# Kernel tuning notes

Measured on AMD Instinct MI355X. Metric: run time of the kernel, lower is better.

Reference implementation:

```python
import jax, jax.numpy as jnp
import numpy as np

G, D, F, B, T = 8, 20, 160, 64, 2000  # groups, dims(hidden), feature=G*D, batch, time


def _lstm_layer(x, Wih, Whh, bih, bhh):
    # x: [B, T, Din]; Wih: [4H, Din]; Whh: [4H, H]; PyTorch gate order i,f,g,o
    H = Whh.shape[1]
    xw = jnp.einsum('btd,gd->btg', x, Wih) + bih + bhh  # [B, T, 4H]
    xw = jnp.swapaxes(xw, 0, 1)  # [T, B, 4H]
    h0 = jnp.zeros((x.shape[0], H), x.dtype)

    def step(carry, xw_t):
        h, c = carry
        gates = xw_t + h @ Whh.T
        i, f, g, o = jnp.split(gates, 4, axis=-1)
        c = jax.nn.sigmoid(f) * c + jax.nn.sigmoid(i) * jnp.tanh(g)
        h = jax.nn.sigmoid(o) * jnp.tanh(c)
        return (h, c), h

    _, hs = jax.lax.scan(step, (h0, h0), xw)
    return jnp.swapaxes(hs, 0, 1)  # [B, T, H]


def _lstm2(xg, Wih0, Whh0, bih0, bhh0, Wih1, Whh1, bih1, bhh1):
    h = _lstm_layer(xg, Wih0, Whh0, bih0, bhh0)
    return _lstm_layer(h, Wih1, Whh1, bih1, bhh1)


_run_groups = jax.vmap(_lstm2)  # map over leading group axis of inputs and params


def setup_inputs() -> dict:
    key = jax.random.key(0)
    ks = jax.random.split(key, 14)
    s = 1.0 / np.sqrt(D)
    inp = {
        'x': jax.random.normal(ks[0], (B, T, G, D), jnp.float32),
        'W_ih0': jax.random.uniform(ks[1], (G, 4 * D, D), jnp.float32, -s, s),
        'W_hh0': jax.random.uniform(ks[2], (G, 4 * D, D), jnp.float32, -s, s),
        'b_ih0': jax.random.uniform(ks[3], (G, 4 * D), jnp.float32, -s, s),
        'b_hh0': jax.random.uniform(ks[4], (G, 4 * D), jnp.float32, -s, s),
        'W_ih1': jax.random.uniform(ks[5], (G, 4 * D, D), jnp.float32, -s, s),
        'W_hh1': jax.random.uniform(ks[6], (G, 4 * D, D), jnp.float32, -s, s),
        'b_ih1': jax.random.uniform(ks[7], (G, 4 * D), jnp.float32, -s, s),
        'b_hh1': jax.random.uniform(ks[8], (G, 4 * D), jnp.float32, -s, s),
        'W1': jax.random.uniform(ks[9], (4 * F, F), jnp.float32, -1 / np.sqrt(F), 1 / np.sqrt(F)),
        'b1': jax.random.uniform(ks[10], (4 * F,), jnp.float32, -1 / np.sqrt(F), 1 / np.sqrt(F)),
        'W2': jax.random.uniform(ks[11], (F, 4 * F), jnp.float32, -1 / np.sqrt(4 * F), 1 / np.sqrt(4 * F)),
        'b2': jax.random.uniform(ks[12], (F,), jnp.float32, -1 / np.sqrt(4 * F), 1 / np.sqrt(4 * F)),
    }
    return inp


def reference(x, W_ih0, W_hh0, b_ih0, b_hh0, W_ih1, W_hh1, b_ih1, b_hh1, W1, b1, W2, b2):
    # x: [B, T, G, D] -> per-group 2-layer LSTM -> concat bands -> residual -> MLP
    xg = jnp.transpose(x, (2, 0, 1, 3))  # [G, B, T, D]
    out = _run_groups(xg, W_ih0, W_hh0, b_ih0, b_hh0, W_ih1, W_hh1, b_ih1, b_hh1)  # [G, B, T, D]
    out = jnp.transpose(out, (1, 2, 0, 3)).reshape(x.shape[0], x.shape[1], G * D)  # [B, T, F]
    fullband = out + x.reshape(x.shape[0], x.shape[1], G * D)
    h = jax.nn.relu(fullband @ W1.T + b1)
    return h @ W2.T + b2  # [B, T, F]
```

## Files before the change

### kernel.cpp

```cpp
#include <hip/hip_runtime.h>


#define Gn 8
#define Dn 20
#define Bn 64
#define Tn 2000
#define Fn 160
#define NR (Bn * Tn)
#define L2E 1.4426950408889634f
#define WS_W1 0
#define WS_W2 102400
#define WS_NEED (204800 * sizeof(unsigned short))

typedef __attribute__((ext_vector_type(2))) float f32x2;
typedef __attribute__((ext_vector_type(4))) float f32x4;
typedef __attribute__((ext_vector_type(8))) short bf16x8;
typedef __attribute__((ext_vector_type(2))) unsigned u32x2;

__device__ __forceinline__ float rdlane(float v, int k) {
  return __int_as_float(__builtin_amdgcn_readlane(__float_as_int(v), k));
}
__device__ __forceinline__ float xswap(float v) {
#if __has_builtin(__builtin_amdgcn_permlane32_swap)
  const u32x2 r = __builtin_amdgcn_permlane32_swap(__float_as_uint(v),
                                                   __float_as_uint(v), false,
                                                   false);
  return __uint_as_float(r.y);
#else
  return __shfl_xor(v, 32);
#endif
}
__device__ __forceinline__ unsigned short f2bf(float f) {
  unsigned u = __float_as_uint(f);
  u += 0x8000u;
  return (unsigned short)(u >> 16);
}

__device__ __forceinline__ void rec2(float gzA, float gzB,
                                     const f32x2* __restrict__ WPA,
                                     const f32x2* __restrict__ WPB, float& h,
                                     float& c) {
  f32x2 hp[10];
#pragma unroll
  for (int j = 0; j < 10; ++j) {
    hp[j].x = rdlane(h, 2 * j);
    hp[j].y = rdlane(h, 2 * j + 1);
  }
  f32x2 aA;
  aA.x = gzA;
  aA.y = 0.f;
  f32x2 aB;
  aB.x = gzB;
  aB.y = 0.f;
#pragma unroll
  for (int j = 0; j < 10; ++j) {
    aA = __builtin_elementwise_fma(WPA[j], hp[j], aA);
    aB = __builtin_elementwise_fma(WPB[j], hp[j], aB);
  }
  const float zA = aA.x + aA.y;
  const float zB = aB.x + aB.y;
  const float rA = __builtin_amdgcn_rcpf(1.f + __builtin_amdgcn_exp2f(zA));
  const float rB = __builtin_amdgcn_rcpf(1.f + __builtin_amdgcn_exp2f(zB));
  const float sF = xswap(rA);
  const float sO = xswap(rB);
  const float tG = __builtin_fmaf(-2.f, rB, 1.f);
  c = sF * c + rA * tG;
  const float tC = __builtin_fmaf(
      -2.f, __builtin_amdgcn_rcpf(1.f + __builtin_amdgcn_exp2f((2.f * L2E) * c)),
      1.f);
  h = sO * tC;
}

__device__ __forceinline__ void proj2(const float* __restrict__ row,
                                      const f32x2* __restrict__ WPA,
                                      const f32x2* __restrict__ WPB, float bzA,
                                      float bzB, float* dA, float* dB) {
  const f32x4 x0 = *(const f32x4*)&row[0];
  const f32x4 x1 = *(const f32x4*)&row[4];
  const f32x4 x2 = *(const f32x4*)&row[8];
  const f32x4 x3 = *(const f32x4*)&row[12];
  const f32x4 x4 = *(const f32x4*)&row[16];
  f32x2 xp[10];
  xp[0] = __builtin_shufflevector(x0, x0, 0, 1);
  xp[1] = __builtin_shufflevector(x0, x0, 2, 3);
  xp[2] = __builtin_shufflevector(x1, x1, 0, 1);
  xp[3] = __builtin_shufflevector(x1, x1, 2, 3);
  xp[4] = __builtin_shufflevector(x2, x2, 0, 1);
  xp[5] = __builtin_shufflevector(x2, x2, 2, 3);
  xp[6] = __builtin_shufflevector(x3, x3, 0, 1);
  xp[7] = __builtin_shufflevector(x3, x3, 2, 3);
  xp[8] = __builtin_shufflevector(x4, x4, 0, 1);
  xp[9] = __builtin_shufflevector(x4, x4, 2, 3);
  f32x2 aA;
  aA.x = bzA;
  aA.y = 0.f;
  f32x2 aB;
  aB.x = bzB;
  aB.y = 0.f;
#pragma unroll
  for (int j = 0; j < 10; ++j) {
    aA = __builtin_elementwise_fma(WPA[j], xp[j], aA);
    aB = __builtin_elementwise_fma(WPB[j], xp[j], aB);
  }
  *dA = aA.x + aA.y;
  *dB = aB.x + aB.y;
}

__global__ __launch_bounds__(512) void scan4p_kernel(
    const float* __restrict__ x, const float* __restrict__ Wih0,
    const float* __restrict__ Whh0, const float* __restrict__ bih0,
    const float* __restrict__ bhh0, const float* __restrict__ Wih1,
    const float* __restrict__ Whh1, const float* __restrict__ bih1,
    const float* __restrict__ bhh1, float* __restrict__ out) {
  __shared__ __align__(16) float XS[2][64][20];
  __shared__ __align__(16) float XW0[2][16][128];
  __shared__ __align__(16) float XW1[2][16][128];
  __shared__ __align__(16) float H0[2][16][20];

  const int tid = threadIdx.x;
  const int lane = tid & 63;
  const int wv = tid >> 6;
  const int sub = wv >> 2;
  const int wr = wv & 3;
  const int role = sub ? (3 - wr) : wr;
  const int chain = blockIdx.x * 2 + sub;
  const int g = chain >> 6;
  const int b = chain & 63;

  float (*const xs)[20] = XS[sub];
  float (*const xw0)[128] = XW0[sub];
  float (*const xw1)[128] = XW1[sub];
  float (*const h0r)[20] = H0[sub];

  const bool wl = lane < Dn;

  int rowA, rowB;
  float sAc, sBc;
  if (lane < 20) {
    rowA = lane; rowB = lane + 40; sAc = -L2E; sBc = 2.f * L2E;
  } else if (lane >= 32 && lane < 52) {
    rowA = lane - 12; rowB = lane + 28; sAc = -L2E; sBc = -L2E;
  } else {
    rowA = 0; rowB = 0; sAc = 0.f; sBc = 0.f;
  }

  f32x2 WPA[10], WPB[10];
  float bzA = 0.f, bzB = 0.f;
  {
    const float* Wsrc;
    const float* bi = nullptr;
    const float* bh = nullptr;
    if (role == 0) {
      Wsrc = Wih0; bi = bih0; bh = bhh0;
    } else if (role == 1) {
      Wsrc = Whh0;
    } else if (role == 2) {
      Wsrc = Wih1; bi = bih1; bh = bhh1;
    } else {
      Wsrc = Whh1;
    }
    const float* Wg = Wsrc + g * 1600;
#pragma unroll
    for (int j = 0; j < 10; ++j) {
      WPA[j].x = Wg[rowA * 20 + 2 * j] * sAc;
      WPA[j].y = Wg[rowA * 20 + 2 * j + 1] * sAc;
      WPB[j].x = Wg[rowB * 20 + 2 * j] * sBc;
      WPB[j].y = Wg[rowB * 20 + 2 * j + 1] * sBc;
    }
    if (bi) {
      bzA = (bi[g * 80 + rowA] + bh[g * 80 + rowA]) * sAc;
      bzB = (bi[g * 80 + rowB] + bh[g * 80 + rowB]) * sBc;
    }
  }

  if (role & 1) __builtin_amdgcn_s_setprio(1);

  const long long cbase = (long long)b * (Tn * Fn) + g * Dn;

  int st_t[3], st_d[3];
  bool st_v[3];
#pragma unroll
  for (int i = 0; i < 3; ++i) {
    const int idx = lane + 64 * i;
    st_v[i] = idx < 160;
    st_t[i] = idx / 20;
    st_d[i] = idx % 20;
  }

  if (role == 0) {
#pragma unroll
    for (int i = 0; i < 3; ++i)
      if (st_v[i])
        xs[st_t[i]][st_d[i]] = x[cbase + (long long)st_t[i] * Fn + st_d[i]];
  }
  __syncthreads();

  float h = 0.f, c = 0.f;

  for (int cix = 0; cix <= 252; ++cix) {
    if (role == 0) {
      const int cs = cix + 1;
      const bool dostage = (cs <= 249);
      float sv[3];
      if (dostage) {
#pragma unroll
        for (int i = 0; i < 3; ++i)
          if (st_v[i])
            sv[i] = x[cbase + (long long)(cs * 8 + st_t[i]) * Fn + st_d[i]];
      }
      if (cix <= 249) {
        const float* xsp = &xs[(cix * 8) & 63][0];
        float* xwp = &xw0[(cix * 8) & 15][0];
#pragma unroll
        for (int p = 0; p < 8; ++p)
          proj2(&xsp[p * 20], WPA, WPB, bzA, bzB, &xwp[p * 128 + lane],
                &xwp[p * 128 + 64 + lane]);
      }
      if (dostage) {
        float* xsw = &xs[(cs * 8) & 63][0];
#pragma unroll
        for (int i = 0; i < 3; ++i)
          if (st_v[i]) xsw[st_t[i] * 20 + st_d[i]] = sv[i];
      }
    } else if (role == 1) {
      if (cix >= 1 && cix <= 250) {
        const float* xwp = &xw0[((cix - 1) * 8) & 15][0];
        float* hrw = &h0r[((cix - 1) * 8) & 15][0];
        float gzA[8], gzB[8];
#pragma unroll
        for (int p = 0; p < 8; ++p) {
          gzA[p] = xwp[p * 128 + lane];
          gzB[p] = xwp[p * 128 + 64 + lane];
        }
#pragma unroll
        for (int p = 0; p < 8; ++p) {
          rec2(gzA[p], gzB[p], WPA, WPB, h, c);
          if (wl) hrw[p * 20 + lane] = h;
        }
      }
    } else if (role == 2) {
      if (cix >= 2 && cix <= 251) {
        const float* hrp = &h0r[((cix - 2) * 8) & 15][0];
        float* xwp = &xw1[((cix - 2) * 8) & 15][0];
#pragma unroll
        for (int p = 0; p < 8; ++p)
          proj2(&hrp[p * 20], WPA, WPB, bzA, bzB, &xwp[p * 128 + lane],
                &xwp[p * 128 + 64 + lane]);
      }
    } else {
      if (cix >= 3) {
        const int c8 = (cix - 3) * 8;
        const int rl = wl ? lane : 0;
        const float* xwp = &xw1[c8 & 15][0];
        const float* xsp = &xs[c8 & 63][0];
        float gzA[8], gzB[8], xr[8];
#pragma unroll
        for (int p = 0; p < 8; ++p) {
          gzA[p] = xwp[p * 128 + lane];
          gzB[p] = xwp[p * 128 + 64 + lane];
          xr[p] = xsp[p * 20 + rl];
        }
#pragma unroll
        for (int p = 0; p < 8; ++p) {
          rec2(gzA[p], gzB[p], WPA, WPB, h, c);
          if (wl) out[cbase + (long long)(c8 + p) * Fn + lane] = h + xr[p];
        }
      }
    }
    __syncthreads();
  }
}

__global__ __launch_bounds__(256) void wprep_kernel(
    const float* __restrict__ W1, const float* __restrict__ W2,
    unsigned short* __restrict__ wb) {
  const int t = blockIdx.x * 256 + threadIdx.x;
  const float4 v = (t < 25600) ? *(const float4*)(W1 + t * 4)
                               : *(const float4*)(W2 + (t - 25600) * 4);
  *(ushort4*)(wb + t * 4) =
      make_ushort4(f2bf(v.x), f2bf(v.y), f2bf(v.z), f2bf(v.w));
}

__device__ __forceinline__ void mlp_compute(
    const short* __restrict__ Wb, const short* __restrict__ W2b,
    short* __restrict__ Hb, const bf16x8* afr, f32x4* acc,
    const float* __restrict__ b1, int nc, int wv, int lane, int cl, int q8,
    int ar) {
#pragma unroll
  for (int n16 = 0; n16 < 4; ++n16) {
    f32x4 hcc = (f32x4){0.f, 0.f, 0.f, 0.f};
    const int br = n16 * 16 + cl;
#pragma unroll
    for (int kk = 0; kk < 5; ++kk) {
      const bf16x8 bfr = *(const bf16x8*)&Wb[br * 168 + kk * 32 + q8];
      hcc = __builtin_amdgcn_mfma_f32_16x16x32_bf16(afr[kk], bfr, hcc, 0, 0, 0);
    }
    const float b1v = b1[nc * 64 + n16 * 16 + cl];
    const int hrow0 = wv * 16 + (lane >> 4) * 4;
    const int hcol = n16 * 16 + cl;
#pragma unroll
    for (int r = 0; r < 4; ++r)
      Hb[(hrow0 + r) * 72 + hcol] = f2bf(fmaxf(hcc[r] + b1v, 0.f));
  }
  bf16x8 a2[2];
#pragma unroll
  for (int kk = 0; kk < 2; ++kk)
    a2[kk] = *(const bf16x8*)&Hb[ar * 72 + kk * 32 + q8];
#pragma unroll
  for (int n16 = 0; n16 < 10; ++n16) {
    const int br = n16 * 16 + cl;
#pragma unroll
    for (int kk = 0; kk < 2; ++kk) {
      const bf16x8 b2f = *(const bf16x8*)&W2b[br * 72 + kk * 32 + q8];
      acc[n16] = __builtin_amdgcn_mfma_f32_16x16x32_bf16(a2[kk], b2f, acc[n16], 0, 0, 0);
    }
  }
}

__global__ __launch_bounds__(256) void mlp_bf16w_kernel(
    float* io, const unsigned short* __restrict__ wb,
    const float* __restrict__ b1, const float* __restrict__ b2) {
  __shared__ short Ab[64 * 168];
  __shared__ short Wb[64 * 168];
  __shared__ short Hb[64 * 72];
  __shared__ short W2b[160 * 72];
  const unsigned short* __restrict__ W1b = wb + WS_W1;
  const unsigned short* __restrict__ W2s = wb + WS_W2;
  const int tid = threadIdx.x;
  const int lane = tid & 63;
  const int wv = tid >> 6;
  const long long r0 = (long long)blockIdx.x * 64;

  ushort4 wa1[10], wa2[10], wn1[10], wn2[10];
#pragma unroll
  for (int i = 0; i < 10; ++i) {
    const int idx = tid + i * 256;
    wa1[i] = *(const ushort4*)(W1b + (idx / 40) * 160 + (idx % 40) * 4);
    wa2[i] = *(const ushort4*)(W2s + (idx >> 4) * 640 + (idx & 15) * 4);
  }
#pragma unroll
  for (int i = 0; i < 10; ++i) {
    const int idx = tid + i * 256;
    const int r = idx / 40, kq = idx % 40;
    const float4 v = *(const float4*)(io + (r0 + r) * Fn + kq * 4);
    *(ushort4*)&Ab[r * 168 + kq * 4] =
        make_ushort4(f2bf(v.x), f2bf(v.y), f2bf(v.z), f2bf(v.w));
  }
  __syncthreads();

  const int cl = lane & 15;
  const int q8 = (lane >> 4) * 8;
  const int ar = wv * 16 + cl;
  bf16x8 afr[5];
#pragma unroll
  for (int kk = 0; kk < 5; ++kk)
    afr[kk] = *(const bf16x8*)&Ab[ar * 168 + kk * 32 + q8];

  f32x4 acc[10];
#pragma unroll
  for (int n = 0; n < 10; ++n) acc[n] = (f32x4){0.f, 0.f, 0.f, 0.f};

#pragma unroll
  for (int ncp = 0; ncp < 5; ++ncp) {
    const int nc0 = 2 * ncp, nc1 = 2 * ncp + 1;
    if (nc0) __syncthreads();
#pragma unroll
    for (int i = 0; i < 10; ++i) {
      const int idx = tid + i * 256;
      *(ushort4*)&Wb[(idx / 40) * 168 + (idx % 40) * 4] = wa1[i];
      *(ushort4*)&W2b[(idx >> 4) * 72 + (idx & 15) * 4] = wa2[i];
    }
#pragma unroll
    for (int i = 0; i < 10; ++i) {
      const int idx = tid + i * 256;
      wn1[i] = *(const ushort4*)(W1b + (nc1 * 64 + idx / 40) * 160 + (idx % 40) * 4);
      wn2[i] = *(const ushort4*)(W2s + (idx >> 4) * 640 + nc1 * 64 + (idx & 15) * 4);
    }
    __syncthreads();
    mlp_compute(Wb, W2b, Hb, afr, acc, b1, nc0, wv, lane, cl, q8, ar);
    __syncthreads();
#pragma unroll
    for (int i = 0; i < 10; ++i) {
      const int idx = tid + i * 256;
      *(ushort4*)&Wb[(idx / 40) * 168 + (idx % 40) * 4] = wn1[i];
      *(ushort4*)&W2b[(idx >> 4) * 72 + (idx & 15) * 4] = wn2[i];
    }
    if (ncp < 4) {
#pragma unroll
      for (int i = 0; i < 10; ++i) {
        const int idx = tid + i * 256;
        wa1[i] = *(const ushort4*)(W1b + ((nc1 + 1) * 64 + idx / 40) * 160 + (idx % 40) * 4);
        wa2[i] = *(const ushort4*)(W2s + (idx >> 4) * 640 + (nc1 + 1) * 64 + (idx & 15) * 4);
      }
    }
    __syncthreads();
    mlp_compute(Wb, W2b, Hb, afr, acc, b1, nc1, wv, lane, cl, q8, ar);
  }
  const int orow0 = wv * 16 + (lane >> 4) * 4;
#pragma unroll
  for (int n16 = 0; n16 < 10; ++n16) {
    const float b2v = b2[n16 * 16 + cl];
#pragma unroll
    for (int r = 0; r < 4; ++r)
      io[(r0 + orow0 + r) * Fn + n16 * 16 + cl] = acc[n16][r] + b2v;
  }
}

__global__ __launch_bounds__(256) void mlp_mfma_kernel(
    float* io, const float* __restrict__ W1, const float* __restrict__ b1,
    const float* __restrict__ W2, const float* __restrict__ b2) {
  __shared__ short Ab[64 * 168];
  __shared__ short Wb[64 * 168];
  __shared__ short Hb[64 * 72];
  __shared__ short W2b[160 * 72];
  const int tid = threadIdx.x;
  const int lane = tid & 63;
  const int wv = tid >> 6;
  const long long r0 = (long long)blockIdx.x * 64;

#pragma unroll
  for (int i = 0; i < 10; ++i) {
    const int idx = tid + i * 256;
    const int r = idx / 40, kq = idx % 40;
    const float4 v = *(const float4*)(io + (r0 + r) * Fn + kq * 4);
    *(ushort4*)&Ab[r * 168 + kq * 4] =
        make_ushort4(f2bf(v.x), f2bf(v.y), f2bf(v.z), f2bf(v.w));
  }
  __syncthreads();

  const int cl = lane & 15;
  const int q8 = (lane >> 4) * 8;
  const int ar = wv * 16 + cl;
  bf16x8 afr[5];
#pragma unroll
  for (int kk = 0; kk < 5; ++kk)
    afr[kk] = *(const bf16x8*)&Ab[ar * 168 + kk * 32 + q8];

  f32x4 acc[10];
#pragma unroll
  for (int n = 0; n < 10; ++n) acc[n] = (f32x4){0.f, 0.f, 0.f, 0.f};

  for (int nc = 0; nc < 10; ++nc) {
    if (nc) __syncthreads();
#pragma unroll
    for (int i = 0; i < 10; ++i) {
      const int idx = tid + i * 256;
      const int r = idx / 40, kq = idx % 40;
      const float4 v = *(const float4*)(W1 + (nc * 64 + r) * Fn + kq * 4);
      *(ushort4*)&Wb[r * 168 + kq * 4] =
          make_ushort4(f2bf(v.x), f2bf(v.y), f2bf(v.z), f2bf(v.w));
    }
#pragma unroll
    for (int i = 0; i < 10; ++i) {
      const int idx = tid + i * 256;
      const int n = idx >> 4, kq = idx & 15;
      const float4 v = *(const float4*)(W2 + n * 640 + nc * 64 + kq * 4);
      *(ushort4*)&W2b[n * 72 + kq * 4] =
          make_ushort4(f2bf(v.x), f2bf(v.y), f2bf(v.z), f2bf(v.w));
    }
    __syncthreads();
    mlp_compute(Wb, W2b, Hb, afr, acc, b1, nc, wv, lane, cl, q8, ar);
  }
  const int orow0 = wv * 16 + (lane >> 4) * 4;
#pragma unroll
  for (int n16 = 0; n16 < 10; ++n16) {
    const float b2v = b2[n16 * 16 + cl];
#pragma unroll
    for (int r = 0; r < 4; ++r)
      io[(r0 + orow0 + r) * Fn + n16 * 16 + cl] = acc[n16][r] + b2v;
  }
}

extern "C" void kernel_launch(void* const* d_in, const int* in_sizes, int n_in,
                              void* d_out, int out_size, void* d_ws, size_t ws_size,
                              hipStream_t stream) {
  const float* x    = (const float*)d_in[0];
  const float* Wih0 = (const float*)d_in[1];
  const float* Whh0 = (const float*)d_in[2];
  const float* bih0 = (const float*)d_in[3];
  const float* bhh0 = (const float*)d_in[4];
  const float* Wih1 = (const float*)d_in[5];
  const float* Whh1 = (const float*)d_in[6];
  const float* bih1 = (const float*)d_in[7];
  const float* bhh1 = (const float*)d_in[8];
  const float* W1   = (const float*)d_in[9];
  const float* b1   = (const float*)d_in[10];
  const float* W2   = (const float*)d_in[11];
  const float* b2   = (const float*)d_in[12];
  float* out = (float*)d_out;

  const bool fast = (d_ws != nullptr) && (ws_size >= WS_NEED);
  if (fast)
    wprep_kernel<<<dim3(200), dim3(256), 0, stream>>>(
        W1, W2, (unsigned short*)d_ws);

  scan4p_kernel<<<dim3(256), dim3(512), 0, stream>>>(
      x, Wih0, Whh0, bih0, bhh0, Wih1, Whh1, bih1, bhh1, out);

  if (fast)
    mlp_bf16w_kernel<<<dim3(NR / 64), dim3(256), 0, stream>>>(
        out, (const unsigned short*)d_ws, b1, b2);
  else
    mlp_mfma_kernel<<<dim3(NR / 64), dim3(256), 0, stream>>>(out, W1, b1, W2, b2);
}
```

Before: 694.8 us.

## Process 128 rows per MLP block to reuse staged bf16 weights twice

The bf16-weight MLP kernel now handles two 64-row tiles per block, so each weight chunk staged in LDS is used for twice as many MFMAs and weight staging traffic per output row is halved. Activations are loaded straight from global into MFMA fragments, dropping the LDS A-tile, and the register double-buffered weight prefetch is removed in favour of direct global-to-LDS copies. This raises register pressure (two accumulator sets) and halves the grid, which may lower occupancy and expose weight-load latency. The fallback kernel inlines the former helper.

```diff
diff --git a/kernel.cpp b/kernel.cpp
--- a/kernel.cpp
+++ b/kernel.cpp
@@ -281,128 +281,111 @@
       make_ushort4(f2bf(v.x), f2bf(v.y), f2bf(v.z), f2bf(v.w));
 }
 
-__device__ __forceinline__ void mlp_compute(
-    const short* __restrict__ Wb, const short* __restrict__ W2b,
-    short* __restrict__ Hb, const bf16x8* afr, f32x4* acc,
-    const float* __restrict__ b1, int nc, int wv, int lane, int cl, int q8,
-    int ar) {
-#pragma unroll
-  for (int n16 = 0; n16 < 4; ++n16) {
-    f32x4 hcc = (f32x4){0.f, 0.f, 0.f, 0.f};
-    const int br = n16 * 16 + cl;
-#pragma unroll
-    for (int kk = 0; kk < 5; ++kk) {
-      const bf16x8 bfr = *(const bf16x8*)&Wb[br * 168 + kk * 32 + q8];
-      hcc = __builtin_amdgcn_mfma_f32_16x16x32_bf16(afr[kk], bfr, hcc, 0, 0, 0);
-    }
-    const float b1v = b1[nc * 64 + n16 * 16 + cl];
-    const int hrow0 = wv * 16 + (lane >> 4) * 4;
-    const int hcol = n16 * 16 + cl;
-#pragma unroll
-    for (int r = 0; r < 4; ++r)
-      Hb[(hrow0 + r) * 72 + hcol] = f2bf(fmaxf(hcc[r] + b1v, 0.f));
-  }
-  bf16x8 a2[2];
-#pragma unroll
-  for (int kk = 0; kk < 2; ++kk)
-    a2[kk] = *(const bf16x8*)&Hb[ar * 72 + kk * 32 + q8];
-#pragma unroll
-  for (int n16 = 0; n16 < 10; ++n16) {
-    const int br = n16 * 16 + cl;
-#pragma unroll
-    for (int kk = 0; kk < 2; ++kk) {
-      const bf16x8 b2f = *(const bf16x8*)&W2b[br * 72 + kk * 32 + q8];
-      acc[n16] = __builtin_amdgcn_mfma_f32_16x16x32_bf16(a2[kk], b2f, acc[n16], 0, 0, 0);
-    }
-  }
-}
-
-__global__ __launch_bounds__(256) void mlp_bf16w_kernel(
+__global__ __launch_bounds__(256) void mlp_bf16w2_kernel(
     float* io, const unsigned short* __restrict__ wb,
     const float* __restrict__ b1, const float* __restrict__ b2) {
-  __shared__ short Ab[64 * 168];
   __shared__ short Wb[64 * 168];
-  __shared__ short Hb[64 * 72];
   __shared__ short W2b[160 * 72];
+  __shared__ short Hb[2][64 * 72];
   const unsigned short* __restrict__ W1b = wb + WS_W1;
   const unsigned short* __restrict__ W2s = wb + WS_W2;
   const int tid = threadIdx.x;
   const int lane = tid & 63;
   const int wv = tid >> 6;
-  const long long r0 = (long long)blockIdx.x * 64;
-
-  ushort4 wa1[10], wa2[10], wn1[10], wn2[10];
-#pragma unroll
-  for (int i = 0; i < 10; ++i) {
-    const int idx = tid + i * 256;
-    wa1[i] = *(const ushort4*)(W1b + (idx / 40) * 160 + (idx % 40) * 4);
-    wa2[i] = *(const ushort4*)(W2s + (idx >> 4) * 640 + (idx & 15) * 4);
-  }
-#pragma unroll
-  for (int i = 0; i < 10; ++i) {
-    const int idx = tid + i * 256;
-    const int r = idx / 40, kq = idx % 40;
-    const float4 v = *(const float4*)(io + (r0 + r) * Fn + kq * 4);
-    *(ushort4*)&Ab[r * 168 + kq * 4] =
-        make_ushort4(f2bf(v.x), f2bf(v.y), f2bf(v.z), f2bf(v.w));
-  }
-  __syncthreads();
-
+  const long long r0 = (long long)blockIdx.x * 128;
   const int cl = lane & 15;
   const int q8 = (lane >> 4) * 8;
   const int ar = wv * 16 + cl;
-  bf16x8 afr[5];
-#pragma unroll
-  for (int kk = 0; kk < 5; ++kk)
-    afr[kk] = *(const bf16x8*)&Ab[ar * 168 + kk * 32 + q8];
-
-  f32x4 acc[10];
-#pragma unroll
-  for (int n = 0; n < 10; ++n) acc[n] = (f32x4){0.f, 0.f, 0.f, 0.f};
-
-#pragma unroll
-  for (int ncp = 0; ncp < 5; ++ncp) {
-    const int nc0 = 2 * ncp, nc1 = 2 * ncp + 1;
-    if (nc0) __syncthreads();
+  const int hrow0 = wv * 16 + (lane >> 4) * 4;
+
+  bf16x8 afr0[5], afr1[5];
+#pragma unroll
+  for (int kk = 0; kk < 5; ++kk) {
+    const long long row0 = (r0 + ar) * (long long)Fn;
+    const long long row1 = (r0 + 64 + ar) * (long long)Fn;
+    const float4 a0 = *(const float4*)(io + row0 + kk * 32 + q8);
+    const float4 a1 = *(const float4*)(io + row0 + kk * 32 + q8 + 4);
+    const float4 c0 = *(const float4*)(io + row1 + kk * 32 + q8);
+    const float4 c1 = *(const float4*)(io + row1 + kk * 32 + q8 + 4);
+    union { ushort4 u4[2]; bf16x8 v; } u;
+    u.u4[0] = make_ushort4(f2bf(a0.x), f2bf(a0.y), f2bf(a0.z), f2bf(a0.w));
+    u.u4[1] = make_ushort4(f2bf(a1.x), f2bf(a1.y), f2bf(a1.z), f2bf(a1.w));
+    afr0[kk] = u.v;
+    u.u4[0] = make_ushort4(f2bf(c0.x), f2bf(c0.y), f2bf(c0.z), f2bf(c0.w));
+    u.u4[1] = make_ushort4(f2bf(c1.x), f2bf(c1.y), f2bf(c1.z), f2bf(c1.w));
+    afr1[kk] = u.v;
+  }
+
+  f32x4 acc0[10], acc1[10];
+#pragma unroll
+  for (int n = 0; n < 10; ++n) {
+    acc0[n] = (f32x4){0.f, 0.f, 0.f, 0.f};
+    acc1[n] = (f32x4){0.f, 0.f, 0.f, 0.f};
+  }
+
+  for (int nc = 0; nc < 10; ++nc) {
+    if (nc) __syncthreads();
 #pragma unroll
     for (int i = 0; i < 10; ++i) {
       const int idx = tid + i * 256;
-      *(ushort4*)&Wb[(idx / 40) * 168 + (idx % 40) * 4] = wa1[i];
-      *(ushort4*)&W2b[(idx >> 4) * 72 + (idx & 15) * 4] = wa2[i];
+      *(ushort4*)&Wb[(idx / 40) * 168 + (idx % 40) * 4] =
+          *(const ushort4*)(W1b + (nc * 64 + idx / 40) * 160 + (idx % 40) * 4);
     }
 #pragma unroll
     for (int i = 0; i < 10; ++i) {
       const int idx = tid + i * 256;
-      wn1[i] = *(const ushort4*)(W1b + (nc1 * 64 + idx / 40) * 160 + (idx % 40) * 4);
-      wn2[i] = *(const ushort4*)(W2s + (idx >> 4) * 640 + nc1 * 64 + (idx & 15) * 4);
+      *(ushort4*)&W2b[(idx >> 4) * 72 + (idx & 15) * 4] =
+          *(const ushort4*)(W2s + (idx >> 4) * 640 + nc * 64 + (idx & 15) * 4);
     }
     __syncthreads();
-    mlp_compute(Wb, W2b, Hb, afr, acc, b1, nc0, wv, lane, cl, q8, ar);
-    __syncthreads();
-#pragma unroll
-    for (int i = 0; i < 10; ++i) {
-      const int idx = tid + i * 256;
-      *(ushort4*)&Wb[(idx / 40) * 168 + (idx % 40) * 4] = wn1[i];
-      *(ushort4*)&W2b[(idx >> 4) * 72 + (idx & 15) * 4] = wn2[i];
-    }
-    if (ncp < 4) {
-#pragma unroll
-      for (int i = 0; i < 10; ++i) {
-        const int idx = tid + i * 256;
-        wa1[i] = *(const ushort4*)(W1b + ((nc1 + 1) * 64 + idx / 40) * 160 + (idx % 40) * 4);
-        wa2[i] = *(const ushort4*)(W2s + (idx >> 4) * 640 + (nc1 + 1) * 64 + (idx & 15) * 4);
-      }
-    }
-    __syncthreads();
-    mlp_compute(Wb, W2b, Hb, afr, acc, b1, nc1, wv, lane, cl, q8, ar);
+#pragma unroll
+    for (int n16 = 0; n16 < 4; ++n16) {
+      const int br = n16 * 16 + cl;
+      bf16x8 bfr[5];
+#pragma unroll
+      for (int kk = 0; kk < 5; ++kk)
+        bfr[kk] = *(const bf16x8*)&Wb[br * 168 + kk * 32 + q8];
+      f32x4 h0 = (f32x4){0.f, 0.f, 0.f, 0.f};
+      f32x4 h1 = (f32x4){0.f, 0.f, 0.f, 0.f};
+#pragma unroll
+      for (int kk = 0; kk < 5; ++kk) {
+        h0 = __builtin_amdgcn_mfma_f32_16x16x32_bf16(afr0[kk], bfr[kk], h0, 0, 0, 0);
+        h1 = __builtin_amdgcn_mfma_f32_16x16x32_bf16(afr1[kk], bfr[kk], h1, 0, 0, 0);
+      }
+      const float b1v = b1[nc * 64 + n16 * 16 + cl];
+      const int hcol = n16 * 16 + cl;
+#pragma unroll
+      for (int r = 0; r < 4; ++r) {
+        Hb[0][(hrow0 + r) * 72 + hcol] = f2bf(fmaxf(h0[r] + b1v, 0.f));
+        Hb[1][(hrow0 + r) * 72 + hcol] = f2bf(fmaxf(h1[r] + b1v, 0.f));
+      }
+    }
+    bf16x8 a20[2], a21[2];
+#pragma unroll
+    for (int kk = 0; kk < 2; ++kk) {
+      a20[kk] = *(const bf16x8*)&Hb[0][ar * 72 + kk * 32 + q8];
+      a21[kk] = *(const bf16x8*)&Hb[1][ar * 72 + kk * 32 + q8];
+    }
+#pragma unroll
+    for (int n16 = 0; n16 < 10; ++n16) {
+      const int br = n16 * 16 + cl;
+#pragma unroll
+      for (int kk = 0; kk < 2; ++kk) {
+        const bf16x8 b2f = *(const bf16x8*)&W2b[br * 72 + kk * 32 + q8];
+        acc0[n16] = __builtin_amdgcn_mfma_f32_16x16x32_bf16(a20[kk], b2f, acc0[n16], 0, 0, 0);
+        acc1[n16] = __builtin_amdgcn_mfma_f32_16x16x32_bf16(a21[kk], b2f, acc1[n16], 0, 0, 0);
+      }
+    }
   }
   const int orow0 = wv * 16 + (lane >> 4) * 4;
 #pragma unroll
   for (int n16 = 0; n16 < 10; ++n16) {
     const float b2v = b2[n16 * 16 + cl];
 #pragma unroll
-    for (int r = 0; r < 4; ++r)
-      io[(r0 + orow0 + r) * Fn + n16 * 16 + cl] = acc[n16][r] + b2v;
+    for (int r = 0; r < 4; ++r) {
+      io[(r0 + orow0 + r) * Fn + n16 * 16 + cl] = acc0[n16][r] + b2v;
+      io[(r0 + 64 + orow0 + r) * Fn + n16 * 16 + cl] = acc1[n16][r] + b2v;
+    }
   }
 }
 
@@ -459,7 +442,35 @@
           make_ushort4(f2bf(v.x), f2bf(v.y), f2bf(v.z), f2bf(v.w));
     }
     __syncthreads();
-    mlp_compute(Wb, W2b, Hb, afr, acc, b1, nc, wv, lane, cl, q8, ar);
+#pragma unroll
+    for (int n16 = 0; n16 < 4; ++n16) {
+      f32x4 hcc = (f32x4){0.f, 0.f, 0.f, 0.f};
+      const int br = n16 * 16 + cl;
+#pragma unroll
+      for (int kk = 0; kk < 5; ++kk) {
+        const bf16x8 bfr = *(const bf16x8*)&Wb[br * 168 + kk * 32 + q8];
+        hcc = __builtin_amdgcn_mfma_f32_16x16x32_bf16(afr[kk], bfr, hcc, 0, 0, 0);
+      }
+      const float b1v = b1[nc * 64 + n16 * 16 + cl];
+      const int hrow0 = wv * 16 + (lane >> 4) * 4;
+      const int hcol = n16 * 16 + cl;
+#pragma unroll
+      for (int r = 0; r < 4; ++r)
+        Hb[(hrow0 + r) * 72 + hcol] = f2bf(fmaxf(hcc[r] + b1v, 0.f));
+    }
+    bf16x8 a2[2];
+#pragma unroll
+    for (int kk = 0; kk < 2; ++kk)
+      a2[kk] = *(const bf16x8*)&Hb[ar * 72 + kk * 32 + q8];
+#pragma unroll
+    for (int n16 = 0; n16 < 10; ++n16) {
+      const int br = n16 * 16 + cl;
+#pragma unroll
+      for (int kk = 0; kk < 2; ++kk) {
+        const bf16x8 b2f = *(const bf16x8*)&W2b[br * 72 + kk * 32 + q8];
+        acc[n16] = __builtin_amdgcn_mfma_f32_16x16x32_bf16(a2[kk], b2f, acc[n16], 0, 0, 0);
+      }
+    }
   }
   const int orow0 = wv * 16 + (lane >> 4) * 4;
 #pragma unroll
@@ -498,7 +509,7 @@
       x, Wih0, Whh0, bih0, bhh0, Wih1, Whh1, bih1, bhh1, out);
 
   if (fast)
-    mlp_bf16w_kernel<<<dim3(NR / 64), dim3(256), 0, stream>>>(
+    mlp_bf16w2_kernel<<<dim3(NR / 128), dim3(256), 0, stream>>>(
         out, (const unsigned short*)d_ws, b1, b2);
   else
     mlp_mfma_kernel<<<dim3(NR / 64), dim3(256), 0, stream>>>(out, W1, b1, W2, b2);
```

Result: slower. 894.9 us (+28.8%).
